# Performance work log

Hardware: AMD Instinct MI355X
Metric: run time of the kernel (lower is better)

## Reference

```python
import jax, jax.numpy as jnp
import numpy as np

B, T, C = 2, 2048, 2048
N_HEAD = 16
N_KV = 4
HEAD = C // N_HEAD  # 128
GROUP = N_HEAD // N_KV


def setup_inputs() -> dict:
    key = jax.random.key(0)
    ks = jax.random.split(key, 5)
    s = 1.0 / np.sqrt(C)
    return {
        "x": jax.random.normal(ks[0], (B, T, C), dtype=jnp.float32),
        "Wq": jax.random.normal(ks[1], (C, C), dtype=jnp.float32) * s,
        "Wk": jax.random.normal(ks[2], (C, N_KV * HEAD), dtype=jnp.float32) * s,
        "Wv": jax.random.normal(ks[3], (C, N_KV * HEAD), dtype=jnp.float32) * s,
        "Wo": jax.random.normal(ks[4], (C, C), dtype=jnp.float32) * s,
    }


def reference(x, Wq, Wk, Wv, Wo):
    Bx, Tx, Cx = x.shape
    q = (x @ Wq).reshape(Bx, Tx, N_HEAD, HEAD).transpose(0, 2, 1, 3)  # (B,H,T,D)
    k = (x @ Wk).reshape(Bx, Tx, N_KV, HEAD).transpose(0, 2, 1, 3)    # (B,KV,T,D)
    v = (x @ Wv).reshape(Bx, Tx, N_KV, HEAD).transpose(0, 2, 1, 3)
    # expand kv heads to query heads (GQA): repeat each kv head GROUP times
    k = jnp.repeat(k, GROUP, axis=1)  # (B,H,T,D)
    v = jnp.repeat(v, GROUP, axis=1)
    scale = 1.0 / np.sqrt(HEAD).astype(np.float32)
    att = jnp.einsum("bhqd,bhkd->bhqk", q, k) * scale  # (B,H,T,T)
    causal = jnp.tril(jnp.ones((Tx, Tx), dtype=bool))
    att = jnp.where(causal[None, None], att, -jnp.inf)
    att = jax.nn.softmax(att, axis=-1)
    y = jnp.einsum("bhqk,bhkd->bhqd", att, v)  # (B,H,T,D)
    y = y.transpose(0, 2, 1, 3).reshape(Bx, Tx, Cx)
    return y @ Wo
```

## Files before the change

kernel.cpp:

```cpp
#include <hip/hip_runtime.h>
#include <cstdint>

typedef unsigned short u16;
typedef unsigned int u32;
typedef __attribute__((ext_vector_type(8))) __bf16 bf16x8;
typedef __attribute__((ext_vector_type(4))) float f32x4;
typedef __attribute__((ext_vector_type(4))) unsigned short u16x4;

#define AS1 __attribute__((address_space(1)))
#define AS3 __attribute__((address_space(3)))

__device__ __forceinline__ void gload16(const void* g, void* l) {
    __builtin_amdgcn_global_load_lds((AS1 void*)g, (AS3 void*)l, 16, 0, 0);
}

__device__ __forceinline__ u16 f2bf(float f) {
    return __builtin_bit_cast(u16, (__bf16)f);
}

__device__ __forceinline__ void store_c(u16* p, float v)   { *p = f2bf(v); }
__device__ __forceinline__ void store_c(float* p, float v) { *p = v; }

__global__ void cvt_bf16(const float* __restrict__ in, u16* __restrict__ out) {
    int i = (blockIdx.x * blockDim.x + threadIdx.x) * 4;
    float4 v = *(const float4*)(in + i);
    u16x4 o = { f2bf(v.x), f2bf(v.y), f2bf(v.z), f2bf(v.w) };
    *(u16x4*)(out + i) = o;
}

__global__ void transpose_cvt(const float* __restrict__ in, u16* __restrict__ out,
                              int R, int Ccols)
{
    __shared__ float tile[32][33];
    int c0 = blockIdx.x * 32, r0 = blockIdx.y * 32;
    int tx = threadIdx.x, ty = threadIdx.y;
#pragma unroll
    for (int i = 0; i < 32; i += 8)
        tile[ty + i][tx] = in[(size_t)(r0 + ty + i) * Ccols + c0 + tx];
    __syncthreads();
#pragma unroll
    for (int i = 0; i < 32; i += 8)
        out[(size_t)(c0 + ty + i) * R + r0 + tx] = f2bf(tile[tx][ty + i]);
}

__global__ void vtrans(const u16* __restrict__ QKV, u16* __restrict__ VT) {
    __shared__ u16 tile[32][33];
    int b = blockIdx.z;
    int c0 = blockIdx.x * 32, r0 = blockIdx.y * 32;
    int tx = threadIdx.x, ty = threadIdx.y;
#pragma unroll
    for (int i = 0; i < 32; i += 8)
        tile[ty + i][tx] = QKV[(size_t)(b * 2048 + r0 + ty + i) * 3072 + 2560 + c0 + tx];
    __syncthreads();
#pragma unroll
    for (int i = 0; i < 32; i += 8)
        VT[(size_t)(b * 512 + c0 + ty + i) * 2048 + r0 + tx] = tile[tx][ty + i];
}

template <typename OT>
__global__ __launch_bounds__(256, 2) void gemm_bt(
    const u16* __restrict__ A, const u16* __restrict__ Bt,
    OT* __restrict__ C, int M, int N, int K)
{
    __shared__ u16 As[128 * 64];
    __shared__ u16 Bs[128 * 64];
    const int tid  = threadIdx.x;
    const int wave = tid >> 6, lane = tid & 63;
    const int quad = lane >> 4, l15 = lane & 15;
    const int bm0 = blockIdx.y * 128, bn0 = blockIdx.x * 128;
    const int wr = (wave >> 1) * 64, wc = (wave & 1) * 64;

    const f32x4 zero = {0.f, 0.f, 0.f, 0.f};
    f32x4 acc[4][4];
#pragma unroll
    for (int i = 0; i < 4; ++i)
#pragma unroll
        for (int j = 0; j < 4; ++j) acc[i][j] = zero;

    const int srow = lane >> 3;
    const int jsw  = ((lane & 7) ^ srow) * 8;

    for (int k0 = 0; k0 < K; k0 += 64) {
#pragma unroll
        for (int i = 0; i < 4; ++i) {
            int c = wave * 4 + i;
            gload16(A  + (size_t)(bm0 + c * 8 + srow) * K + k0 + jsw, As + c * 512);
            gload16(Bt + (size_t)(bn0 + c * 8 + srow) * K + k0 + jsw, Bs + c * 512);
        }
        __syncthreads();
#pragma unroll
        for (int ks = 0; ks < 2; ++ks) {
            bf16x8 a[4], b[4];
#pragma unroll
            for (int t = 0; t < 4; ++t) {
                int rd = ((ks * 4 + quad) ^ (l15 & 7)) * 8;
                a[t] = *(const bf16x8*)(As + (wr + t * 16 + l15) * 64 + rd);
                b[t] = *(const bf16x8*)(Bs + (wc + t * 16 + l15) * 64 + rd);
            }
#pragma unroll
            for (int i = 0; i < 4; ++i)
#pragma unroll
                for (int j = 0; j < 4; ++j)
                    acc[i][j] = __builtin_amdgcn_mfma_f32_16x16x32_bf16(a[i], b[j], acc[i][j], 0, 0, 0);
        }
        __syncthreads();
    }
#pragma unroll
    for (int i = 0; i < 4; ++i) {
        int grow = bm0 + wr + i * 16 + quad * 4;
#pragma unroll
        for (int j = 0; j < 4; ++j) {
            int gcol = bn0 + wc + j * 16 + l15;
#pragma unroll
            for (int r = 0; r < 4; ++r)
                store_c(&C[(size_t)(grow + r) * N + gcol], acc[i][j][r]);
        }
    }
}

__global__ __launch_bounds__(512, 4) void attn(
    const u16* __restrict__ QKV, const u16* __restrict__ VT, u16* __restrict__ Y)
{
    __shared__ u16 Ks[2][64 * 128];
    __shared__ u16 Vs[128 * 64];
    __shared__ u16 Ps[8][16 * 72];

    const int tid  = threadIdx.x;
    const int wave = tid >> 6, lane = tid & 63;
    const int quad = lane >> 4, l15 = lane & 15;
    const int w4 = wave & 3;
    int pi = blockIdx.x;
    const int bh = blockIdx.y;
    if (bh >= 16) pi = 15 - pi;
    const int qtA = 2 * pi, qtB = 2 * pi + 1;
    const int b = bh >> 4, h = bh & 15, kv = h >> 2;

    const int myqt = (wave < 4) ? qtA : qtB;
    const int q0 = myqt * 64 + w4 * 16;

    bf16x8 aq[4];
    {
        const u16* qp = QKV + (size_t)(b * 2048 + q0 + l15) * 3072 + h * 128 + quad * 8;
#pragma unroll
        for (int ks = 0; ks < 4; ++ks) aq[ks] = *(const bf16x8*)(qp + ks * 32);
    }

    bf16x8 ones;
#pragma unroll
    for (int i = 0; i < 8; ++i) ones[i] = __builtin_bit_cast(__bf16, (u16)0x3F80);

    const f32x4 zero = {0.f, 0.f, 0.f, 0.f};
    f32x4 o[9];
#pragma unroll
    for (int i = 0; i < 9; ++i) o[i] = zero;

    const u16* Kbase = QKV + 2048 + kv * 128;
    const u16* Vbase = VT + (size_t)((b * 4 + kv) * 128) * 2048;
    u16* pw = &Ps[wave][0];

    const int kr = lane >> 4;
    const int vr = lane >> 3;
    const int vjs = ((lane & 7) ^ vr) * 8;

    auto stageK = [&](int buf, int kt) {
#pragma unroll
        for (int i = 0; i < 2; ++i) {
            int ci = wave * 2 + i;
            int krow = ci * 4 + kr;
            int kjs = ((lane & 15) ^ (krow & 15)) * 8;
            gload16(Kbase + (size_t)(b * 2048 + kt * 64 + krow) * 3072 + kjs,
                    &Ks[buf][ci * 512]);
        }
    };
    auto stageV = [&](int kt) {
#pragma unroll
        for (int i = 0; i < 2; ++i) {
            int ci = wave * 2 + i;
            int vrow = ci * 8 + vr;
            gload16(Vbase + (size_t)vrow * 2048 + kt * 64 + vjs, &Vs[ci * 512]);
        }
    };

    const float c1 = 0.12752817f;
    const float c2 = 28.85390082f;

    stageK(0, 0);
    __syncthreads();

    for (int kt = 0; kt <= qtB; ++kt) {
        const int cur = kt & 1;
        stageV(kt);
        const bool pre = (kt < qtB);
        if (pre) stageK(cur ^ 1, kt + 1);

        const bool act = (kt <= myqt);
        const u16* Ksc = &Ks[cur][0];

        if (act) {
            f32x4 s[4];
#pragma unroll
            for (int i = 0; i < 4; ++i) s[i] = zero;
            __builtin_amdgcn_s_setprio(1);
#pragma unroll
            for (int ks = 0; ks < 4; ++ks)
#pragma unroll
                for (int kc = 0; kc < 4; ++kc) {
                    bf16x8 bk = *(const bf16x8*)(Ksc + (kc * 16 + l15) * 128 + (((ks * 4 + quad) ^ l15) * 8));
                    s[kc] = __builtin_amdgcn_mfma_f32_16x16x32_bf16(aq[ks], bk, s[kc], 0, 0, 0);
                }
            __builtin_amdgcn_s_setprio(0);
            const bool diag = (kt == myqt);
#pragma unroll
            for (int kc = 0; kc < 4; ++kc)
#pragma unroll
                for (int r = 0; r < 4; ++r) {
                    float arg = fmaf(s[kc][r], c1, -c2);
                    if (diag && (kc * 16 + l15) > (w4 * 16 + quad * 4 + r)) arg = -10000.f;
                    float p = __builtin_amdgcn_exp2f(arg);
                    pw[(quad * 4 + r) * 72 + kc * 16 + l15] = f2bf(p);
                }
            asm volatile("" ::: "memory");
        }

        if (pre) asm volatile("s_waitcnt vmcnt(2)" ::: "memory");
        else     asm volatile("s_waitcnt vmcnt(0)" ::: "memory");
        __builtin_amdgcn_s_barrier();

        if (act) {
            __builtin_amdgcn_s_setprio(1);
#pragma unroll
            for (int ks2 = 0; ks2 < 2; ++ks2) {
                bf16x8 pa = *(const bf16x8*)(pw + l15 * 72 + ks2 * 32 + quad * 8);
#pragma unroll
                for (int d = 0; d < 8; ++d) {
                    bf16x8 bv = *(const bf16x8*)(Vs + (d * 16 + l15) * 64 + (((ks2 * 4 + quad) ^ (l15 & 7)) * 8));
                    o[d] = __builtin_amdgcn_mfma_f32_16x16x32_bf16(pa, bv, o[d], 0, 0, 0);
                }
                o[8] = __builtin_amdgcn_mfma_f32_16x16x32_bf16(pa, ones, o[8], 0, 0, 0);
            }
            __builtin_amdgcn_s_setprio(0);
        }

        asm volatile("s_waitcnt vmcnt(0) lgkmcnt(0)" ::: "memory");
        __builtin_amdgcn_s_barrier();
    }

    float inv[4];
#pragma unroll
    for (int r = 0; r < 4; ++r) inv[r] = 1.0f / o[8][r];
#pragma unroll
    for (int d = 0; d < 8; ++d)
#pragma unroll
        for (int r = 0; r < 4; ++r)
            Y[(size_t)(b * 2048 + q0 + quad * 4 + r) * 2048 + h * 128 + d * 16 + l15] =
                f2bf(o[d][r] * inv[r]);
}

extern "C" void kernel_launch(void* const* d_in, const int* in_sizes, int n_in,
                              void* d_out, int out_size, void* d_ws, size_t ws_size,
                              hipStream_t stream)
{
    const float* x  = (const float*)d_in[0];
    const float* Wq = (const float*)d_in[1];
    const float* Wk = (const float*)d_in[2];
    const float* Wv = (const float*)d_in[3];
    const float* Wo = (const float*)d_in[4];
    float* out = (float*)d_out;

    char* ws = (char*)d_ws;
    u16* xb    = (u16*)ws; ws += (size_t)4096 * 2048 * 2;
    u16* WqkvT = (u16*)ws; ws += (size_t)3072 * 2048 * 2;
    u16* WoT   = (u16*)ws; ws += (size_t)2048 * 2048 * 2;
    u16* QKVb  = (u16*)ws; ws += (size_t)4096 * 3072 * 2;
    u16* VT    = (u16*)ws;
    u16* Y     = xb;

    dim3 tblk(32, 8, 1);
    cvt_bf16<<<8192, 256, 0, stream>>>(x, xb);
    transpose_cvt<<<dim3(64, 64, 1), tblk, 0, stream>>>(Wq, WqkvT, 2048, 2048);
    transpose_cvt<<<dim3(16, 64, 1), tblk, 0, stream>>>(Wk, WqkvT + (size_t)2048 * 2048, 2048, 512);
    transpose_cvt<<<dim3(16, 64, 1), tblk, 0, stream>>>(Wv, WqkvT + (size_t)2560 * 2048, 2048, 512);
    transpose_cvt<<<dim3(64, 64, 1), tblk, 0, stream>>>(Wo, WoT, 2048, 2048);

    gemm_bt<u16><<<dim3(24, 32, 1), 256, 0, stream>>>(xb, WqkvT, QKVb, 4096, 3072, 2048);

    vtrans<<<dim3(16, 64, 2), tblk, 0, stream>>>(QKVb, VT);

    attn<<<dim3(16, 32, 1), 512, 0, stream>>>(QKVb, VT, Y);

    gemm_bt<float><<<dim3(16, 32, 1), 256, 0, stream>>>(Y, WoT, out, 4096, 2048, 2048);
}
```

Before: 267.2 us.

## Repartition attention waves to share P tile across four waves per query tile

Instead of each wave owning 16 query rows against all 64 keys, each wave of a four-wave group now computes S for all 64 query rows against 16 keys, writes into a shared 64x72 P tile, then computes O for all 64 rows over 32 head dims. Each wave loads only its K slice and V columns once, reusing them across four query sub-tiles. This is meant to cut redundant LDS reads of K and V. In exchange it needs 16 Q fragments in registers, an lgkmcnt wait before the barrier, and a shared-memory exchange of the row sums at the end.

```diff
diff --git a/kernel.cpp b/kernel.cpp
--- a/kernel.cpp
+++ b/kernel.cpp
@@ -123,7 +123,7 @@
 {
     __shared__ u16 Ks[2][64 * 128];
     __shared__ u16 Vs[128 * 64];
-    __shared__ u16 Ps[8][16 * 72];
+    __shared__ u16 Ps[2][64 * 72];
 
     const int tid  = threadIdx.x;
     const int wave = tid >> 6, lane = tid & 63;
@@ -136,13 +136,15 @@
     const int b = bh >> 4, h = bh & 15, kv = h >> 2;
 
     const int myqt = (wave < 4) ? qtA : qtB;
-    const int q0 = myqt * 64 + w4 * 16;
-
-    bf16x8 aq[4];
+
+    bf16x8 aq[4][4];
     {
-        const u16* qp = QKV + (size_t)(b * 2048 + q0 + l15) * 3072 + h * 128 + quad * 8;
-#pragma unroll
-        for (int ks = 0; ks < 4; ++ks) aq[ks] = *(const bf16x8*)(qp + ks * 32);
+        const u16* qp = QKV + (size_t)(b * 2048 + myqt * 64 + l15) * 3072 + h * 128 + quad * 8;
+#pragma unroll
+        for (int qr = 0; qr < 4; ++qr)
+#pragma unroll
+            for (int ks = 0; ks < 4; ++ks)
+                aq[qr][ks] = *(const bf16x8*)(qp + (size_t)qr * 16 * 3072 + ks * 32);
     }
 
     bf16x8 ones;
@@ -150,13 +152,16 @@
     for (int i = 0; i < 8; ++i) ones[i] = __builtin_bit_cast(__bf16, (u16)0x3F80);
 
     const f32x4 zero = {0.f, 0.f, 0.f, 0.f};
-    f32x4 o[9];
-#pragma unroll
-    for (int i = 0; i < 9; ++i) o[i] = zero;
+    f32x4 o[4][2];
+#pragma unroll
+    for (int qr = 0; qr < 4; ++qr)
+#pragma unroll
+        for (int j = 0; j < 2; ++j) o[qr][j] = zero;
+    f32x4 o8 = zero;
 
     const u16* Kbase = QKV + 2048 + kv * 128;
     const u16* Vbase = VT + (size_t)((b * 4 + kv) * 128) * 2048;
-    u16* pw = &Ps[wave][0];
+    u16* pg = &Ps[wave >> 2][0];
 
     const int kr = lane >> 4;
     const int vr = lane >> 3;
@@ -200,43 +205,52 @@
             f32x4 s[4];
 #pragma unroll
             for (int i = 0; i < 4; ++i) s[i] = zero;
+            bf16x8 bk[4];
+#pragma unroll
+            for (int ks = 0; ks < 4; ++ks)
+                bk[ks] = *(const bf16x8*)(Ksc + (w4 * 16 + l15) * 128 + (((ks * 4 + quad) ^ l15) * 8));
             __builtin_amdgcn_s_setprio(1);
 #pragma unroll
             for (int ks = 0; ks < 4; ++ks)
 #pragma unroll
-                for (int kc = 0; kc < 4; ++kc) {
-                    bf16x8 bk = *(const bf16x8*)(Ksc + (kc * 16 + l15) * 128 + (((ks * 4 + quad) ^ l15) * 8));
-                    s[kc] = __builtin_amdgcn_mfma_f32_16x16x32_bf16(aq[ks], bk, s[kc], 0, 0, 0);
-                }
+                for (int qr = 0; qr < 4; ++qr)
+                    s[qr] = __builtin_amdgcn_mfma_f32_16x16x32_bf16(aq[qr][ks], bk[ks], s[qr], 0, 0, 0);
             __builtin_amdgcn_s_setprio(0);
             const bool diag = (kt == myqt);
 #pragma unroll
-            for (int kc = 0; kc < 4; ++kc)
+            for (int qr = 0; qr < 4; ++qr)
 #pragma unroll
                 for (int r = 0; r < 4; ++r) {
-                    float arg = fmaf(s[kc][r], c1, -c2);
-                    if (diag && (kc * 16 + l15) > (w4 * 16 + quad * 4 + r)) arg = -10000.f;
+                    float arg = fmaf(s[qr][r], c1, -c2);
+                    if (diag && (w4 * 16 + l15) > (qr * 16 + quad * 4 + r)) arg = -10000.f;
                     float p = __builtin_amdgcn_exp2f(arg);
-                    pw[(quad * 4 + r) * 72 + kc * 16 + l15] = f2bf(p);
+                    pg[(qr * 16 + quad * 4 + r) * 72 + w4 * 16 + l15] = f2bf(p);
                 }
             asm volatile("" ::: "memory");
         }
 
-        if (pre) asm volatile("s_waitcnt vmcnt(2)" ::: "memory");
-        else     asm volatile("s_waitcnt vmcnt(0)" ::: "memory");
+        if (pre) asm volatile("s_waitcnt vmcnt(2) lgkmcnt(0)" ::: "memory");
+        else     asm volatile("s_waitcnt vmcnt(0) lgkmcnt(0)" ::: "memory");
         __builtin_amdgcn_s_barrier();
 
         if (act) {
             __builtin_amdgcn_s_setprio(1);
 #pragma unroll
             for (int ks2 = 0; ks2 < 2; ++ks2) {
-                bf16x8 pa = *(const bf16x8*)(pw + l15 * 72 + ks2 * 32 + quad * 8);
-#pragma unroll
-                for (int d = 0; d < 8; ++d) {
-                    bf16x8 bv = *(const bf16x8*)(Vs + (d * 16 + l15) * 64 + (((ks2 * 4 + quad) ^ (l15 & 7)) * 8));
-                    o[d] = __builtin_amdgcn_mfma_f32_16x16x32_bf16(pa, bv, o[d], 0, 0, 0);
-                }
-                o[8] = __builtin_amdgcn_mfma_f32_16x16x32_bf16(pa, ones, o[8], 0, 0, 0);
+                bf16x8 pa[4];
+#pragma unroll
+                for (int qr = 0; qr < 4; ++qr)
+                    pa[qr] = *(const bf16x8*)(pg + (qr * 16 + l15) * 72 + ks2 * 32 + quad * 8);
+                bf16x8 bv[2];
+#pragma unroll
+                for (int j = 0; j < 2; ++j)
+                    bv[j] = *(const bf16x8*)(Vs + ((w4 * 2 + j) * 16 + l15) * 64 + (((ks2 * 4 + quad) ^ (l15 & 7)) * 8));
+#pragma unroll
+                for (int qr = 0; qr < 4; ++qr)
+#pragma unroll
+                    for (int j = 0; j < 2; ++j)
+                        o[qr][j] = __builtin_amdgcn_mfma_f32_16x16x32_bf16(pa[qr], bv[j], o[qr][j], 0, 0, 0);
+                o8 = __builtin_amdgcn_mfma_f32_16x16x32_bf16(pa[w4], ones, o8, 0, 0, 0);
             }
             __builtin_amdgcn_s_setprio(0);
         }
@@ -245,15 +259,25 @@
         __builtin_amdgcn_s_barrier();
     }
 
-    float inv[4];
-#pragma unroll
-    for (int r = 0; r < 4; ++r) inv[r] = 1.0f / o[8][r];
-#pragma unroll
-    for (int d = 0; d < 8; ++d)
+    float* dl = (float*)&Ps[0][0];
+    const int gofs = (wave < 4) ? 0 : 64;
+    if (l15 == 0) {
 #pragma unroll
         for (int r = 0; r < 4; ++r)
-            Y[(size_t)(b * 2048 + q0 + quad * 4 + r) * 2048 + h * 128 + d * 16 + l15] =
-                f2bf(o[d][r] * inv[r]);
+            dl[gofs + w4 * 16 + quad * 4 + r] = o8[r];
+    }
+    __syncthreads();
+
+#pragma unroll
+    for (int qr = 0; qr < 4; ++qr)
+#pragma unroll
+        for (int r = 0; r < 4; ++r) {
+            float invv = 1.0f / dl[gofs + qr * 16 + quad * 4 + r];
+#pragma unroll
+            for (int j = 0; j < 2; ++j)
+                Y[(size_t)(b * 2048 + myqt * 64 + qr * 16 + quad * 4 + r) * 2048
+                  + h * 128 + (w4 * 2 + j) * 16 + l15] = f2bf(o[qr][j][r] * invv);
+        }
 }
 
 extern "C" void kernel_launch(void* const* d_in, const int* in_sizes, int n_in,
```

Result: slower. 603.3 us (+125.8%).
